# Performance work log

Hardware: AMD Instinct MI355X
Metric: run time of the kernel (lower is better)

The kernel has to match this reference:

```python
import jax, jax.numpy as jnp
import numpy as np

B, N = 16, 4096
N_IN, E_OUT = 128, 128          # inpt_dim[1], outp_dim[0]
OUT_N = 128                     # outp_dim[1]
G_DIM, CTXT_DIM = 64, 64
NODE_IN = E_OUT + N_IN          # 256, pre_ln size
CTXT_IN = G_DIM + CTXT_DIM      # 128
HID_F, HID_A = 256, 128
N_HEADS = 4
HEAD_DIM = OUT_N // N_HEADS     # 32
LN_EPS = 1e-5


def _init_w(key, fan_in, fan_out):
    return jax.random.normal(key, (fan_in, fan_out), jnp.float32) / np.float32(np.sqrt(fan_in))


def setup_inputs() -> dict:
    key = jax.random.key(0)
    ks = jax.random.split(key, 10)
    nodes = jax.random.normal(ks[0], (B, N, N_IN), jnp.float32)
    pooled_edges = jax.random.normal(ks[1], (B, N, E_OUT), jnp.float32)
    # variable-length graphs: valid prefix per graph (at least half the nodes)
    lengths = jax.random.randint(ks[2], (B,), N // 2, N + 1)
    mask = jnp.arange(N)[None, :] < lengths[:, None]
    globs = jax.random.normal(ks[3], (B, G_DIM), jnp.float32)
    ctxt = jax.random.normal(ks[4], (B, CTXT_DIM), jnp.float32)
    return {
        "nodes": nodes,
        "pooled_edges": pooled_edges,
        "mask": mask,
        "globs": globs,
        "ctxt": ctxt,
        "ln_g": jnp.ones((NODE_IN,), jnp.float32),
        "ln_b": jnp.zeros((NODE_IN,), jnp.float32),
        "feat_w1": _init_w(ks[5], NODE_IN + CTXT_IN, HID_F),
        "feat_b1": jnp.zeros((HID_F,), jnp.float32),
        "feat_w2": _init_w(ks[6], HID_F, OUT_N),
        "feat_b2": jnp.zeros((OUT_N,), jnp.float32),
        "attn_w1": _init_w(ks[7], NODE_IN + CTXT_IN, HID_A),
        "attn_b1": jnp.zeros((HID_A,), jnp.float32),
        "attn_w2": _init_w(ks[8], HID_A, N_HEADS),
        "attn_b2": jnp.zeros((N_HEADS,), jnp.float32),
    }


def _mlp(x, w1, b1, w2, b2):
    # DenseNetwork: one hidden block with LeakyReLU ("lrlu"), linear output
    h = jax.nn.leaky_relu(x @ w1 + b1)
    return h @ w2 + b2


def reference(nodes, pooled_edges, mask, globs, ctxt, ln_g, ln_b,
              feat_w1, feat_b1, feat_w2, feat_b2,
              attn_w1, attn_b1, attn_w2, attn_b2):
    # nodes = cat([graph.nodes, pooled_edges]) -> pre-LayerNorm
    x = jnp.concatenate([nodes, pooled_edges], axis=-1)           # [B,N,256]
    mu = jnp.mean(x, axis=-1, keepdims=True)
    var = jnp.var(x, axis=-1, keepdims=True)
    x = (x - mu) * jax.lax.rsqrt(var + LN_EPS) * ln_g + ln_b

    # high-level context broadcast to every node
    hl = jnp.concatenate([globs, ctxt], axis=-1)                   # [B,128]
    hl = jnp.broadcast_to(hl[:, None, :], (x.shape[0], x.shape[1], hl.shape[-1]))
    xin = jnp.concatenate([x, hl], axis=-1)                        # [B,N,384]

    # attention net with -inf padding, softmax over node axis (dim=-2)
    logits = _mlp(xin, attn_w1, attn_b1, attn_w2, attn_b2)          # [B,N,H]
    logits = jnp.where(mask[..., None], logits, -jnp.inf)
    w = jax.nn.softmax(logits, axis=1) / np.float32(np.sqrt(OUT_N))
    w = jnp.where(mask[..., None], w, 0.0)

    # feature net with 0 padding + residual (same_size)
    feats = _mlp(xin, feat_w1, feat_b1, feat_w2, feat_b2)           # [B,N,128]
    feats = jnp.where(mask[..., None], feats, 0.0)
    new_nodes = feats + nodes

    # expand per-head weights across head_dim, flatten, weighted node pooling
    w_full = jnp.repeat(w, HEAD_DIM, axis=-1)                       # [B,N,128]
    pooled = jnp.sum(new_nodes * w_full, axis=1)                    # [B,128]
    return (new_nodes, pooled)
```

## Files before the change

kernel.cpp:

```cpp
#include <hip/hip_runtime.h>
#include <stdint.h>

typedef unsigned short u16;
typedef unsigned char  u8;
typedef unsigned int   u32;
typedef __attribute__((ext_vector_type(8))) short bf16x8;
typedef __attribute__((ext_vector_type(4))) float f32x4;

static __device__ __forceinline__ float bf2f(u32 u) {
    union { u32 i; float f; } x; x.i = u << 16; return x.f;
}
static __device__ __forceinline__ u16 f2bf(float f) {
    union { u32 i; float f; } x; x.f = f;
    return (u16)((x.i + 0x7fffu + ((x.i >> 16) & 1u)) >> 16);
}
static __device__ __forceinline__ u32 packbf(float a, float b) {
    return (u32)f2bf(a) | ((u32)f2bf(b) << 16);
}
static __device__ __forceinline__ float ldf(const void* p, int i, int isf32) {
    return isf32 ? ((const float*)p)[i] : bf2f(((const u16*)p)[i]);
}
static __device__ __forceinline__ bool mvalid(const void* mask, int g, int mi32) {
    return mi32 ? (((const int*)mask)[g] != 0) : (((const u8*)mask)[g] != 0);
}

#define NTOT 65536
#define SXLD 264
#define SHLD 136
#define PVLD 144

__global__ __launch_bounds__(256) void k0_prep(
    const void* __restrict__ feat_w1, const void* __restrict__ attn_w1,
    const void* __restrict__ feat_b1, const void* __restrict__ attn_b1,
    const void* __restrict__ feat_w2, const void* __restrict__ attn_w2,
    const void* __restrict__ globs, const void* __restrict__ ctxt,
    const void* __restrict__ ln_g,
    u16* __restrict__ W1t, u16* __restrict__ W2t, u16* __restrict__ aw2t,
    float* __restrict__ hlc)
{
    __shared__ u16 tile[64][66];
    __shared__ float hl[128];
    const int isf32 = (((const u32*)ln_g)[0] == 0x3F800000u);
    const int bid = blockIdx.x;
    const int t = threadIdx.x;

    if (bid < 24) {
        int jt = bid >> 2, kt = bid & 3;
        int j0 = jt * 64, k0 = kt * 64;
        int jj = t & 63, kq = t >> 6;
#pragma unroll
        for (int r = 0; r < 16; r++) {
            int kk = r * 4 + kq;
            int j = j0 + jj;
            float v = (j < 256) ? ldf(feat_w1, (k0 + kk) * 256 + j, isf32)
                                : ldf(attn_w1, (k0 + kk) * 128 + (j - 256), isf32);
            tile[kk][jj] = f2bf(v);
        }
        __syncthreads();
        int kk2 = t & 63, jq = t >> 6;
#pragma unroll
        for (int r = 0; r < 16; r++) {
            int jj2 = r * 4 + jq;
            W1t[(size_t)(j0 + jj2) * 256 + k0 + kk2] = tile[kk2][jj2];
        }
    } else if (bid < 32) {
        int id2 = bid - 24;
        int ct2 = id2 >> 2, kt = id2 & 3;
        int c0 = ct2 * 64, k0 = kt * 64;
        int cc = t & 63, kq = t >> 6;
#pragma unroll
        for (int r = 0; r < 16; r++) {
            int kk = r * 4 + kq;
            tile[kk][cc] = f2bf(ldf(feat_w2, (k0 + kk) * 128 + c0 + cc, isf32));
        }
        __syncthreads();
        int kk2 = t & 63, cq = t >> 6;
#pragma unroll
        for (int r = 0; r < 16; r++) {
            int cc2 = r * 4 + cq;
            W2t[(size_t)(c0 + cc2) * 256 + k0 + kk2] = tile[kk2][cc2];
        }
    } else if (bid == 32) {
#pragma unroll
        for (int i = 0; i < 8; i++) {
            int e = i * 256 + t;
            int n = e >> 7, k = e & 127;
            aw2t[e] = (n < 4) ? f2bf(ldf(attn_w2, k * 4 + n, isf32)) : (u16)0;
        }
    } else {
        int b = bid - 33;
        if (t < 64)       hl[t] = ldf(globs, b * 64 + t, isf32);
        else if (t < 128) hl[t] = ldf(ctxt, b * 64 + (t - 64), isf32);
        __syncthreads();
        {
            float s = ldf(feat_b1, t, isf32);
#pragma unroll 8
            for (int c = 0; c < 128; c++)
                s += hl[c] * ldf(feat_w1, (256 + c) * 256 + t, isf32);
            hlc[b * 384 + t] = s;
        }
        if (t < 128) {
            float s = ldf(attn_b1, t, isf32);
#pragma unroll 8
            for (int c = 0; c < 128; c++)
                s += hl[c] * ldf(attn_w1, (256 + c) * 128 + t, isf32);
            hlc[b * 384 + 256 + t] = s;
        }
    }
}

__global__ __launch_bounds__(256, 3) void k_mega(
    const void* __restrict__ nodes, const void* __restrict__ edges,
    const void* __restrict__ ln_g, const void* __restrict__ ln_b,
    const u16* __restrict__ W1t, const u16* __restrict__ W2t,
    const u16* __restrict__ aw2t, const float* __restrict__ hlc,
    const void* __restrict__ attn_b2, const void* __restrict__ feat_b2,
    const void* __restrict__ mask,
    float* __restrict__ pv, void* __restrict__ outp)
{
    __shared__ __align__(16) u16 sX[64 * SXLD];
    __shared__ __align__(16) u16 sH[64 * SHLD];
    __shared__ float sG[256], sBt[256];
    __shared__ float sL[64][4];
    const int t = threadIdx.x;
    const int g0 = blockIdx.x * 64;
    const int b = g0 >> 12;
    const int isf32 = (((const u32*)ln_g)[0] == 0x3F800000u);
    const int mi32  = (((const u32*)mask)[0] == 1u);

    sG[t]  = ldf(ln_g, t, isf32);
    sBt[t] = ldf(ln_b, t, isf32);
    __syncthreads();

#pragma unroll
    for (int half = 0; half < 2; half++) {
        const int r = half * 32 + (t >> 3), q8 = t & 7;
        u32 pk[16];
#pragma unroll
        for (int j = 0; j < 4; j++) {
            int c = q8 + j * 8;
            if (isf32) {
                const float* src = (c < 16)
                    ? ((const float*)nodes + (size_t)(g0 + r) * 128 + c * 8)
                    : ((const float*)edges + (size_t)(g0 + r) * 128 + (c - 16) * 8);
                float4 v0 = ((const float4*)src)[0];
                float4 v1 = ((const float4*)src)[1];
                pk[4 * j]     = packbf(v0.x, v0.y);
                pk[4 * j + 1] = packbf(v0.z, v0.w);
                pk[4 * j + 2] = packbf(v1.x, v1.y);
                pk[4 * j + 3] = packbf(v1.z, v1.w);
            } else {
                const u16* src = (c < 16)
                    ? ((const u16*)nodes + (size_t)(g0 + r) * 128 + c * 8)
                    : ((const u16*)edges + (size_t)(g0 + r) * 128 + (c - 16) * 8);
                uint4 v = ((const uint4*)src)[0];
                pk[4 * j] = v.x; pk[4 * j + 1] = v.y;
                pk[4 * j + 2] = v.z; pk[4 * j + 3] = v.w;
            }
        }
        float s = 0.f, q = 0.f;
#pragma unroll
        for (int i = 0; i < 16; i++) {
            float lo = bf2f(pk[i] & 0xffffu), hi = bf2f(pk[i] >> 16);
            s += lo + hi; q += lo * lo + hi * hi;
        }
        s += __shfl_xor(s, 1, 64); s += __shfl_xor(s, 2, 64); s += __shfl_xor(s, 4, 64);
        q += __shfl_xor(q, 1, 64); q += __shfl_xor(q, 2, 64); q += __shfl_xor(q, 4, 64);
        float mu = s * (1.f / 256.f);
        float var = q * (1.f / 256.f) - mu * mu;
        float rs = rsqrtf(var + 1e-5f);
#pragma unroll
        for (int j = 0; j < 4; j++) {
            int c = q8 + j * 8;
            u32 ow[4];
#pragma unroll
            for (int k2 = 0; k2 < 4; k2++) {
                int col = c * 8 + k2 * 2;
                u32 w2 = pk[4 * j + k2];
                float y0 = (bf2f(w2 & 0xffffu) - mu) * rs * sG[col]     + sBt[col];
                float y1 = (bf2f(w2 >> 16)     - mu) * rs * sG[col + 1] + sBt[col + 1];
                ow[k2] = packbf(y0, y1);
            }
            *(uint4*)&sX[r * SXLD + c * 8] = make_uint4(ow[0], ow[1], ow[2], ow[3]);
        }
    }
    __syncthreads();

    const int w = t >> 6, l = t & 63;
    const int lr = l & 15, lq = l >> 4;
    const float ab2 = (lr < 4) ? ldf(attn_b2, lr, isf32) : 0.f;
    const float fb2_0 = ldf(feat_b2, w * 32 + lr, isf32);
    const float fb2_1 = ldf(feat_b2, w * 32 + 16 + lr, isf32);
    float* pvb = pv + (size_t)blockIdx.x * PVLD;

    f32x4 acc2[4][2];
#pragma unroll
    for (int rt = 0; rt < 4; rt++)
#pragma unroll
        for (int ct = 0; ct < 2; ct++) acc2[rt][ct] = (f32x4){0.f, 0.f, 0.f, 0.f};

    float nv[4][2][4];
    bool  mrow[4][4];

    const int order[3] = {2, 0, 1};
#pragma unroll
    for (int oi = 0; oi < 3; oi++) {
        const int nt = order[oi];

        float hbv[2];
#pragma unroll
        for (int ct = 0; ct < 2; ct++)
            hbv[ct] = hlc[b * 384 + nt * 128 + w * 32 + ct * 16 + lr];

        f32x4 acc1[4][2];
#pragma unroll
        for (int rt = 0; rt < 4; rt++)
#pragma unroll
            for (int ct = 0; ct < 2; ct++) acc1[rt][ct] = (f32x4){0.f, 0.f, 0.f, 0.f};

        const u16* Wp = W1t + (size_t)(nt * 128 + w * 32 + lr) * 256;
#pragma unroll
        for (int kh = 0; kh < 2; kh++) {
            bf16x8 bW[4][2];
#pragma unroll
            for (int kk = 0; kk < 4; kk++)
#pragma unroll
                for (int ct = 0; ct < 2; ct++)
                    bW[kk][ct] = *(const bf16x8*)(Wp + ct * 16 * 256 + (kh * 4 + kk) * 32 + lq * 8);
#pragma unroll
            for (int kk = 0; kk < 4; kk++) {
                bf16x8 aF[4];
#pragma unroll
                for (int rt = 0; rt < 4; rt++)
                    aF[rt] = *(const bf16x8*)&sX[(rt * 16 + lr) * SXLD + ((kh * 4 + kk) * 4 + lq) * 8];
#pragma unroll
                for (int rt = 0; rt < 4; rt++)
#pragma unroll
                    for (int ct = 0; ct < 2; ct++)
                        acc1[rt][ct] = __builtin_amdgcn_mfma_f32_16x16x32_bf16(aF[rt], bW[kk][ct], acc1[rt][ct], 0, 0, 0);
            }
        }

        __syncthreads();
#pragma unroll
        for (int rt = 0; rt < 4; rt++)
#pragma unroll
            for (int ct = 0; ct < 2; ct++)
#pragma unroll
                for (int reg = 0; reg < 4; reg++) {
                    int row = rt * 16 + lq * 4 + reg;
                    int col = w * 32 + ct * 16 + lr;
                    float hv = acc1[rt][ct][reg] + hbv[ct];
                    hv = (hv >= 0.f) ? hv : 0.01f * hv;
                    sH[row * SHLD + col] = f2bf(hv);
                }

        if (oi == 1) {
            const int row = l;
            const bool vld = mvalid(mask, g0 + row, mi32);
            float lg = sL[row][w];
            float x = vld ? lg : -1e30f;
#pragma unroll
            for (int o = 1; o < 64; o <<= 1) x = fmaxf(x, __shfl_xor(x, o, 64));
            float e = vld ? expf(lg - x) : 0.f;
            sL[row][w] = e;
            float sgm = e;
#pragma unroll
            for (int o = 1; o < 64; o <<= 1) sgm += __shfl_xor(sgm, o, 64);
            if (l == 0) { pvb[128 + w] = sgm; pvb[132 + w] = x; }
        }
        __syncthreads();

        if (nt == 2) {
            f32x4 accL = (f32x4){0.f, 0.f, 0.f, 0.f};
#pragma unroll
            for (int kk = 0; kk < 4; kk++) {
                bf16x8 aF = *(const bf16x8*)&sH[(w * 16 + lr) * SHLD + (kk * 4 + lq) * 8];
                bf16x8 bF = *(const bf16x8*)(aw2t + lr * 128 + kk * 32 + lq * 8);
                accL = __builtin_amdgcn_mfma_f32_16x16x32_bf16(aF, bF, accL, 0, 0, 0);
            }
            if (lr < 4) {
#pragma unroll
                for (int reg = 0; reg < 4; reg++)
                    sL[w * 16 + lq * 4 + reg][lr] = accL[reg] + ab2;
            }
        } else {
            if (oi == 2) {
#pragma unroll
                for (int rt = 0; rt < 4; rt++)
#pragma unroll
                    for (int reg = 0; reg < 4; reg++) {
                        int row = rt * 16 + lq * 4 + reg;
                        mrow[rt][reg] = mvalid(mask, g0 + row, mi32);
#pragma unroll
                        for (int ct = 0; ct < 2; ct++)
                            nv[rt][ct][reg] = ldf(nodes,
                                (g0 + row) * 128 + w * 32 + ct * 16 + lr, isf32);
                    }
            }
            const u16* W2p = W2t + (size_t)(w * 32 + lr) * 256 + nt * 128;
            bf16x8 bW2[4][2];
#pragma unroll
            for (int kk = 0; kk < 4; kk++)
#pragma unroll
                for (int ct = 0; ct < 2; ct++)
                    bW2[kk][ct] = *(const bf16x8*)(W2p + ct * 16 * 256 + kk * 32 + lq * 8);
#pragma unroll
            for (int kk = 0; kk < 4; kk++) {
                bf16x8 aF[4];
#pragma unroll
                for (int rt = 0; rt < 4; rt++)
                    aF[rt] = *(const bf16x8*)&sH[(rt * 16 + lr) * SHLD + (kk * 4 + lq) * 8];
#pragma unroll
                for (int rt = 0; rt < 4; rt++)
#pragma unroll
                    for (int ct = 0; ct < 2; ct++)
                        acc2[rt][ct] = __builtin_amdgcn_mfma_f32_16x16x32_bf16(aF[rt], bW2[kk][ct], acc2[rt][ct], 0, 0, 0);
            }
        }
    }

    float pc0 = 0.f, pc1 = 0.f;
#pragma unroll
    for (int rt = 0; rt < 4; rt++)
#pragma unroll
        for (int ct = 0; ct < 2; ct++)
#pragma unroll
            for (int reg = 0; reg < 4; reg++) {
                int row = rt * 16 + lq * 4 + reg;
                int col = w * 32 + ct * 16 + lr;
                int g = g0 + row;
                float v = acc2[rt][ct][reg] + (ct ? fb2_1 : fb2_0);
                v = mrow[rt][reg] ? v : 0.f;
                v += nv[rt][ct][reg];
                size_t idx = (size_t)g * 128 + col;
                if (isf32) ((float*)outp)[idx] = v;
                else       ((u16*)outp)[idx] = f2bf(v);
                float e = sL[row][w];
                if (ct) pc1 += e * v; else pc0 += e * v;
            }
    pc0 += __shfl_xor(pc0, 16, 64); pc0 += __shfl_xor(pc0, 32, 64);
    pc1 += __shfl_xor(pc1, 16, 64); pc1 += __shfl_xor(pc1, 32, 64);
    if (lq == 0) {
        pvb[w * 32 + lr]      = pc0;
        pvb[w * 32 + 16 + lr] = pc1;
    }
}

__global__ __launch_bounds__(256) void k_final(
    const float* __restrict__ pv, const void* __restrict__ ln_g,
    void* __restrict__ outbase)
{
    __shared__ float sm[64][4], ss[64][4], se[64][4];
    __shared__ float sZ[4];
    __shared__ float part[2][128];
    const int b = blockIdx.x;
    const int t = threadIdx.x;
    const int isf32 = (((const u32*)ln_g)[0] == 0x3F800000u);
    const float* pvb = pv + (size_t)b * 64 * PVLD;

#pragma unroll
    for (int i = t; i < 512; i += 256) {
        int rec = i >> 3, j = i & 7;
        float x = pvb[(size_t)rec * PVLD + 128 + j];
        if (j < 4) ss[rec][j] = x;
        else       sm[rec][j - 4] = x;
    }
    __syncthreads();

    {
        const int h = t >> 6, i = t & 63;
        float m = sm[i][h];
#pragma unroll
        for (int o = 1; o < 64; o <<= 1) m = fmaxf(m, __shfl_xor(m, o, 64));
        float e = expf(sm[i][h] - m);
        se[i][h] = e;
        float z = e * ss[i][h];
#pragma unroll
        for (int o = 1; o < 64; o <<= 1) z += __shfl_xor(z, o, 64);
        if (i == 0) sZ[h] = z;
    }
    __syncthreads();

    {
        const int c = t & 127, half = t >> 7;
        const int h = c >> 5;
        float acc = 0.f;
#pragma unroll 8
        for (int j = 0; j < 32; j++) {
            int rec = half * 32 + j;
            acc += se[rec][h] * pvb[(size_t)rec * PVLD + c];
        }
        part[half][c] = acc;
    }
    __syncthreads();
    if (t < 128) {
        float p = (part[0][t] + part[1][t]) * (0.08838834764831845f / sZ[t >> 5]);
        size_t off = (size_t)NTOT * 128 + (size_t)b * 128 + t;
        if (isf32) ((float*)outbase)[off] = p;
        else       ((u16*)outbase)[off] = f2bf(p);
    }
}

extern "C" void kernel_launch(void* const* d_in, const int* in_sizes, int n_in,
                              void* d_out, int out_size, void* d_ws, size_t ws_size,
                              hipStream_t stream)
{
    const void* nodes   = d_in[0];
    const void* edges   = d_in[1];
    const void* mask    = d_in[2];
    const void* globs   = d_in[3];
    const void* ctxt    = d_in[4];
    const void* ln_g    = d_in[5];
    const void* ln_b    = d_in[6];
    const void* feat_w1 = d_in[7];
    const void* feat_b1 = d_in[8];
    const void* feat_w2 = d_in[9];
    const void* feat_b2 = d_in[10];
    const void* attn_w1 = d_in[11];
    const void* attn_b1 = d_in[12];
    const void* attn_w2 = d_in[13];
    const void* attn_b2 = d_in[14];

    char* ws = (char*)d_ws;
    u16*   W1t    = (u16*)ws;   ws += (size_t)384 * 256 * 2;
    u16*   W2t    = (u16*)ws;   ws += (size_t)128 * 256 * 2;
    u16*   aw2t   = (u16*)ws;   ws += (size_t)16 * 128 * 2;
    float* hlc    = (float*)ws; ws += (size_t)16 * 384 * 4;
    float* pv     = (float*)ws; ws += (size_t)1024 * PVLD * 4;

    k0_prep <<<dim3(49),   dim3(256), 0, stream>>>(feat_w1, attn_w1, feat_b1, attn_b1,
                                                   feat_w2, attn_w2, globs, ctxt, ln_g,
                                                   W1t, W2t, aw2t, hlc);
    k_mega  <<<dim3(1024), dim3(256), 0, stream>>>(nodes, edges, ln_g, ln_b, W1t, W2t,
                                                   aw2t, hlc, attn_b2, feat_b2, mask,
                                                   pv, d_out);
    k_final <<<dim3(16),   dim3(256), 0, stream>>>(pv, ln_g, d_out);
}
```

Measured before the change: 198.0 us.

## Double waves per block and fold final pooling into last-arriving block

The main kernel now runs 512 threads per block with 8 waves, each owning 16 output columns instead of 32. This halves per-wave accumulator and weight-fragment registers, aiming for more latency hiding. The separate final reduction kernel is removed. The last block of each graph, found with an atomic counter and thread fences, now does the softmax-normalised pooling, saving one kernel launch. The cost is the atomic and fence overhead, a serial tail in the last block of each graph, and attention-logit MFMA work limited to half the waves.

```diff
diff --git a/kernel.cpp b/kernel.cpp
--- a/kernel.cpp
+++ b/kernel.cpp
@@ -36,7 +36,7 @@
     const void* __restrict__ globs, const void* __restrict__ ctxt,
     const void* __restrict__ ln_g,
     u16* __restrict__ W1t, u16* __restrict__ W2t, u16* __restrict__ aw2t,
-    float* __restrict__ hlc)
+    float* __restrict__ hlc, int* __restrict__ cnt)
 {
     __shared__ u16 tile[64][66];
     __shared__ float hl[128];
@@ -81,6 +81,7 @@
             W2t[(size_t)(c0 + cc2) * 256 + k0 + kk2] = tile[kk2][cc2];
         }
     } else if (bid == 32) {
+        if (t < 16) cnt[t] = 0;
 #pragma unroll
         for (int i = 0; i < 8; i++) {
             int e = i * 256 + t;
@@ -109,32 +110,31 @@
     }
 }
 
-__global__ __launch_bounds__(256, 3) void k_mega(
+__global__ __launch_bounds__(512, 4) void k_mega(
     const void* __restrict__ nodes, const void* __restrict__ edges,
     const void* __restrict__ ln_g, const void* __restrict__ ln_b,
     const u16* __restrict__ W1t, const u16* __restrict__ W2t,
     const u16* __restrict__ aw2t, const float* __restrict__ hlc,
     const void* __restrict__ attn_b2, const void* __restrict__ feat_b2,
     const void* __restrict__ mask,
-    float* __restrict__ pv, void* __restrict__ outp)
+    float* __restrict__ pv, int* __restrict__ cnt, void* __restrict__ outp)
 {
     __shared__ __align__(16) u16 sX[64 * SXLD];
     __shared__ __align__(16) u16 sH[64 * SHLD];
     __shared__ float sG[256], sBt[256];
     __shared__ float sL[64][4];
+    __shared__ int sFin;
     const int t = threadIdx.x;
     const int g0 = blockIdx.x * 64;
     const int b = g0 >> 12;
     const int isf32 = (((const u32*)ln_g)[0] == 0x3F800000u);
     const int mi32  = (((const u32*)mask)[0] == 1u);
 
-    sG[t]  = ldf(ln_g, t, isf32);
-    sBt[t] = ldf(ln_b, t, isf32);
-    __syncthreads();
-
-#pragma unroll
-    for (int half = 0; half < 2; half++) {
-        const int r = half * 32 + (t >> 3), q8 = t & 7;
+    if (t < 256) { sG[t] = ldf(ln_g, t, isf32); sBt[t] = ldf(ln_b, t, isf32); }
+    __syncthreads();
+
+    {
+        const int r = t >> 3, q8 = t & 7;
         u32 pk[16];
 #pragma unroll
         for (int j = 0; j < 4; j++) {
@@ -188,45 +188,35 @@
 
     const int w = t >> 6, l = t & 63;
     const int lr = l & 15, lq = l >> 4;
+    const int cb = w * 16;
     const float ab2 = (lr < 4) ? ldf(attn_b2, lr, isf32) : 0.f;
-    const float fb2_0 = ldf(feat_b2, w * 32 + lr, isf32);
-    const float fb2_1 = ldf(feat_b2, w * 32 + 16 + lr, isf32);
+    const float fb2 = ldf(feat_b2, cb + lr, isf32);
     float* pvb = pv + (size_t)blockIdx.x * PVLD;
 
-    f32x4 acc2[4][2];
-#pragma unroll
-    for (int rt = 0; rt < 4; rt++)
-#pragma unroll
-        for (int ct = 0; ct < 2; ct++) acc2[rt][ct] = (f32x4){0.f, 0.f, 0.f, 0.f};
-
-    float nv[4][2][4];
+    f32x4 acc2[4];
+#pragma unroll
+    for (int rt = 0; rt < 4; rt++) acc2[rt] = (f32x4){0.f, 0.f, 0.f, 0.f};
+
+    float nv[4][4];
     bool  mrow[4][4];
 
     const int order[3] = {2, 0, 1};
 #pragma unroll
     for (int oi = 0; oi < 3; oi++) {
         const int nt = order[oi];
-
-        float hbv[2];
-#pragma unroll
-        for (int ct = 0; ct < 2; ct++)
-            hbv[ct] = hlc[b * 384 + nt * 128 + w * 32 + ct * 16 + lr];
-
-        f32x4 acc1[4][2];
-#pragma unroll
-        for (int rt = 0; rt < 4; rt++)
-#pragma unroll
-            for (int ct = 0; ct < 2; ct++) acc1[rt][ct] = (f32x4){0.f, 0.f, 0.f, 0.f};
-
-        const u16* Wp = W1t + (size_t)(nt * 128 + w * 32 + lr) * 256;
+        const float hbv = hlc[b * 384 + nt * 128 + cb + lr];
+
+        f32x4 acc1[4];
+#pragma unroll
+        for (int rt = 0; rt < 4; rt++) acc1[rt] = (f32x4){0.f, 0.f, 0.f, 0.f};
+
+        const u16* Wp = W1t + (size_t)(nt * 128 + cb + lr) * 256;
 #pragma unroll
         for (int kh = 0; kh < 2; kh++) {
-            bf16x8 bW[4][2];
+            bf16x8 bW[4];
 #pragma unroll
             for (int kk = 0; kk < 4; kk++)
-#pragma unroll
-                for (int ct = 0; ct < 2; ct++)
-                    bW[kk][ct] = *(const bf16x8*)(Wp + ct * 16 * 256 + (kh * 4 + kk) * 32 + lq * 8);
+                bW[kk] = *(const bf16x8*)(Wp + (kh * 4 + kk) * 32 + lq * 8);
 #pragma unroll
             for (int kk = 0; kk < 4; kk++) {
                 bf16x8 aF[4];
@@ -235,9 +225,7 @@
                     aF[rt] = *(const bf16x8*)&sX[(rt * 16 + lr) * SXLD + ((kh * 4 + kk) * 4 + lq) * 8];
 #pragma unroll
                 for (int rt = 0; rt < 4; rt++)
-#pragma unroll
-                    for (int ct = 0; ct < 2; ct++)
-                        acc1[rt][ct] = __builtin_amdgcn_mfma_f32_16x16x32_bf16(aF[rt], bW[kk][ct], acc1[rt][ct], 0, 0, 0);
+                    acc1[rt] = __builtin_amdgcn_mfma_f32_16x16x32_bf16(aF[rt], bW[kk], acc1[rt], 0, 0, 0);
             }
         }
 
@@ -245,17 +233,14 @@
 #pragma unroll
         for (int rt = 0; rt < 4; rt++)
 #pragma unroll
-            for (int ct = 0; ct < 2; ct++)
-#pragma unroll
-                for (int reg = 0; reg < 4; reg++) {
-                    int row = rt * 16 + lq * 4 + reg;
-                    int col = w * 32 + ct * 16 + lr;
-                    float hv = acc1[rt][ct][reg] + hbv[ct];
-                    hv = (hv >= 0.f) ? hv : 0.01f * hv;
-                    sH[row * SHLD + col] = f2bf(hv);
-                }
-
-        if (oi == 1) {
+            for (int reg = 0; reg < 4; reg++) {
+                int row = rt * 16 + lq * 4 + reg;
+                float hv = acc1[rt][reg] + hbv;
+                hv = (hv >= 0.f) ? hv : 0.01f * hv;
+                sH[row * SHLD + cb + lr] = f2bf(hv);
+            }
+
+        if (oi == 1 && w < 4) {
             const int row = l;
             const bool vld = mvalid(mask, g0 + row, mi32);
             float lg = sL[row][w];
@@ -272,17 +257,19 @@
         __syncthreads();
 
         if (nt == 2) {
-            f32x4 accL = (f32x4){0.f, 0.f, 0.f, 0.f};
-#pragma unroll
-            for (int kk = 0; kk < 4; kk++) {
-                bf16x8 aF = *(const bf16x8*)&sH[(w * 16 + lr) * SHLD + (kk * 4 + lq) * 8];
-                bf16x8 bF = *(const bf16x8*)(aw2t + lr * 128 + kk * 32 + lq * 8);
-                accL = __builtin_amdgcn_mfma_f32_16x16x32_bf16(aF, bF, accL, 0, 0, 0);
-            }
-            if (lr < 4) {
-#pragma unroll
-                for (int reg = 0; reg < 4; reg++)
-                    sL[w * 16 + lq * 4 + reg][lr] = accL[reg] + ab2;
+            if (w < 4) {
+                f32x4 accL = (f32x4){0.f, 0.f, 0.f, 0.f};
+#pragma unroll
+                for (int kk = 0; kk < 4; kk++) {
+                    bf16x8 aF = *(const bf16x8*)&sH[(w * 16 + lr) * SHLD + (kk * 4 + lq) * 8];
+                    bf16x8 bF = *(const bf16x8*)(aw2t + lr * 128 + kk * 32 + lq * 8);
+                    accL = __builtin_amdgcn_mfma_f32_16x16x32_bf16(aF, bF, accL, 0, 0, 0);
+                }
+                if (lr < 4) {
+#pragma unroll
+                    for (int reg = 0; reg < 4; reg++)
+                        sL[w * 16 + lq * 4 + reg][lr] = accL[reg] + ab2;
+                }
             }
         } else {
             if (oi == 2) {
@@ -292,19 +279,14 @@
                     for (int reg = 0; reg < 4; reg++) {
                         int row = rt * 16 + lq * 4 + reg;
                         mrow[rt][reg] = mvalid(mask, g0 + row, mi32);
-#pragma unroll
-                        for (int ct = 0; ct < 2; ct++)
-                            nv[rt][ct][reg] = ldf(nodes,
-                                (g0 + row) * 128 + w * 32 + ct * 16 + lr, isf32);
+                        nv[rt][reg] = ldf(nodes, (g0 + row) * 128 + cb + lr, isf32);
                     }
             }
-            const u16* W2p = W2t + (size_t)(w * 32 + lr) * 256 + nt * 128;
-            bf16x8 bW2[4][2];
+            const u16* W2p = W2t + (size_t)(cb + lr) * 256 + nt * 128;
+            bf16x8 bW2[4];
 #pragma unroll
             for (int kk = 0; kk < 4; kk++)
-#pragma unroll
-                for (int ct = 0; ct < 2; ct++)
-                    bW2[kk][ct] = *(const bf16x8*)(W2p + ct * 16 * 256 + kk * 32 + lq * 8);
+                bW2[kk] = *(const bf16x8*)(W2p + kk * 32 + lq * 8);
 #pragma unroll
             for (int kk = 0; kk < 4; kk++) {
                 bf16x8 aF[4];
@@ -313,92 +295,82 @@
                     aF[rt] = *(const bf16x8*)&sH[(rt * 16 + lr) * SHLD + (kk * 4 + lq) * 8];
 #pragma unroll
                 for (int rt = 0; rt < 4; rt++)
-#pragma unroll
-                    for (int ct = 0; ct < 2; ct++)
-                        acc2[rt][ct] = __builtin_amdgcn_mfma_f32_16x16x32_bf16(aF[rt], bW2[kk][ct], acc2[rt][ct], 0, 0, 0);
-            }
-        }
-    }
-
-    float pc0 = 0.f, pc1 = 0.f;
+                    acc2[rt] = __builtin_amdgcn_mfma_f32_16x16x32_bf16(aF[rt], bW2[kk], acc2[rt], 0, 0, 0);
+            }
+        }
+    }
+
+    float pc = 0.f;
 #pragma unroll
     for (int rt = 0; rt < 4; rt++)
 #pragma unroll
-        for (int ct = 0; ct < 2; ct++)
-#pragma unroll
-            for (int reg = 0; reg < 4; reg++) {
-                int row = rt * 16 + lq * 4 + reg;
-                int col = w * 32 + ct * 16 + lr;
-                int g = g0 + row;
-                float v = acc2[rt][ct][reg] + (ct ? fb2_1 : fb2_0);
-                v = mrow[rt][reg] ? v : 0.f;
-                v += nv[rt][ct][reg];
-                size_t idx = (size_t)g * 128 + col;
-                if (isf32) ((float*)outp)[idx] = v;
-                else       ((u16*)outp)[idx] = f2bf(v);
-                float e = sL[row][w];
-                if (ct) pc1 += e * v; else pc0 += e * v;
-            }
-    pc0 += __shfl_xor(pc0, 16, 64); pc0 += __shfl_xor(pc0, 32, 64);
-    pc1 += __shfl_xor(pc1, 16, 64); pc1 += __shfl_xor(pc1, 32, 64);
-    if (lq == 0) {
-        pvb[w * 32 + lr]      = pc0;
-        pvb[w * 32 + 16 + lr] = pc1;
-    }
-}
-
-__global__ __launch_bounds__(256) void k_final(
-    const float* __restrict__ pv, const void* __restrict__ ln_g,
-    void* __restrict__ outbase)
-{
-    __shared__ float sm[64][4], ss[64][4], se[64][4];
-    __shared__ float sZ[4];
-    __shared__ float part[2][128];
-    const int b = blockIdx.x;
-    const int t = threadIdx.x;
-    const int isf32 = (((const u32*)ln_g)[0] == 0x3F800000u);
-    const float* pvb = pv + (size_t)b * 64 * PVLD;
-
-#pragma unroll
-    for (int i = t; i < 512; i += 256) {
-        int rec = i >> 3, j = i & 7;
-        float x = pvb[(size_t)rec * PVLD + 128 + j];
-        if (j < 4) ss[rec][j] = x;
-        else       sm[rec][j - 4] = x;
-    }
-    __syncthreads();
+        for (int reg = 0; reg < 4; reg++) {
+            int row = rt * 16 + lq * 4 + reg;
+            int g = g0 + row;
+            float v = acc2[rt][reg] + fb2;
+            v = mrow[rt][reg] ? v : 0.f;
+            v += nv[rt][reg];
+            size_t idx = (size_t)g * 128 + cb + lr;
+            if (isf32) ((float*)outp)[idx] = v;
+            else       ((u16*)outp)[idx] = f2bf(v);
+            pc += sL[row][w >> 1] * v;
+        }
+    pc += __shfl_xor(pc, 16, 64); pc += __shfl_xor(pc, 32, 64);
+    if (lq == 0) pvb[cb + lr] = pc;
+
+    __threadfence();
+    if (t == 0) sFin = (atomicAdd(&cnt[b], 1) == 63);
+    __syncthreads();
+    if (!sFin) return;
+    __threadfence();
+
+    float* fsm  = (float*)sX;
+    float* fss  = fsm + 256;
+    float* fse  = fss + 256;
+    float* fsZ  = fse + 256;
+    float* fpart = fsZ + 4;
+    const float* pvbase = pv + (size_t)(b * 64) * PVLD;
 
     {
+        int rec = t >> 3, j = t & 7;
+        float x = pvbase[(size_t)rec * PVLD + 128 + j];
+        if (j < 4) fss[rec * 4 + j] = x;
+        else       fsm[rec * 4 + (j - 4)] = x;
+    }
+    __syncthreads();
+
+    if (t < 256) {
         const int h = t >> 6, i = t & 63;
-        float m = sm[i][h];
+        float m = fsm[i * 4 + h];
 #pragma unroll
         for (int o = 1; o < 64; o <<= 1) m = fmaxf(m, __shfl_xor(m, o, 64));
-        float e = expf(sm[i][h] - m);
-        se[i][h] = e;
-        float z = e * ss[i][h];
+        float e = expf(fsm[i * 4 + h] - m);
+        fse[i * 4 + h] = e;
+        float z = e * fss[i * 4 + h];
 #pragma unroll
         for (int o = 1; o < 64; o <<= 1) z += __shfl_xor(z, o, 64);
-        if (i == 0) sZ[h] = z;
+        if (i == 0) fsZ[h] = z;
     }
     __syncthreads();
 
     {
-        const int c = t & 127, half = t >> 7;
+        const int c = t & 127, qq = t >> 7;
         const int h = c >> 5;
         float acc = 0.f;
-#pragma unroll 8
-        for (int j = 0; j < 32; j++) {
-            int rec = half * 32 + j;
-            acc += se[rec][h] * pvb[(size_t)rec * PVLD + c];
-        }
-        part[half][c] = acc;
+#pragma unroll
+        for (int j = 0; j < 16; j++) {
+            int rec = qq * 16 + j;
+            acc += fse[rec * 4 + h] * pvbase[(size_t)rec * PVLD + c];
+        }
+        fpart[qq * 128 + c] = acc;
     }
     __syncthreads();
     if (t < 128) {
-        float p = (part[0][t] + part[1][t]) * (0.08838834764831845f / sZ[t >> 5]);
+        float p = (fpart[t] + fpart[128 + t] + fpart[256 + t] + fpart[384 + t])
+                  * (0.08838834764831845f / fsZ[t >> 5]);
         size_t off = (size_t)NTOT * 128 + (size_t)b * 128 + t;
-        if (isf32) ((float*)outbase)[off] = p;
-        else       ((u16*)outbase)[off] = f2bf(p);
+        if (isf32) ((float*)outp)[off] = p;
+        else       ((u16*)outp)[off] = f2bf(p);
     }
 }
 
@@ -428,12 +400,12 @@
     u16*   aw2t   = (u16*)ws;   ws += (size_t)16 * 128 * 2;
     float* hlc    = (float*)ws; ws += (size_t)16 * 384 * 4;
     float* pv     = (float*)ws; ws += (size_t)1024 * PVLD * 4;
+    int*   cnt    = (int*)ws;   ws += 16 * 4;
 
     k0_prep <<<dim3(49),   dim3(256), 0, stream>>>(feat_w1, attn_w1, feat_b1, attn_b1,
                                                    feat_w2, attn_w2, globs, ctxt, ln_g,
-                                                   W1t, W2t, aw2t, hlc);
-    k_mega  <<<dim3(1024), dim3(256), 0, stream>>>(nodes, edges, ln_g, ln_b, W1t, W2t,
+                                                   W1t, W2t, aw2t, hlc, cnt);
+    k_mega  <<<dim3(1024), dim3(512), 0, stream>>>(nodes, edges, ln_g, ln_b, W1t, W2t,
                                                    aw2t, hlc, attn_b2, feat_b2, mask,
-                                                   pv, d_out);
-    k_final <<<dim3(16),   dim3(256), 0, stream>>>(pv, ln_g, d_out);
-}
+                                                   pv, cnt, d_out);
+}
```

Measured after the change: 454.0 us. 129% more time.

## Prefetch next W1 tile before barrier and split final pooling per head

Applied to the files above, without the earlier changes.

The main kernel now issues global loads of the first half of each W1 column block before the LayerNorm barrier and prefetches the next block's first half while the current block finishes, so weight-fetch latency overlaps with MFMA work and the barrier. The final reduction kernel is split into 64 blocks (one per batch and head) instead of 16, which spreads the softmax-combine work across more CUs. This raises register pressure in the mega kernel because of the extra prefetched fragments, which could cut occupancy.

```diff
diff --git a/kernel.cpp b/kernel.cpp
--- a/kernel.cpp
+++ b/kernel.cpp
@@ -184,7 +184,6 @@
             *(uint4*)&sX[r * SXLD + c * 8] = make_uint4(ow[0], ow[1], ow[2], ow[3]);
         }
     }
-    __syncthreads();
 
     const int w = t >> 6, l = t & 63;
     const int lr = l & 15, lq = l >> 4;
@@ -193,6 +192,17 @@
     const float fb2_1 = ldf(feat_b2, w * 32 + 16 + lr, isf32);
     float* pvb = pv + (size_t)blockIdx.x * PVLD;
 
+    bf16x8 bW0[4][2];
+    {
+        const u16* Wf = W1t + (size_t)(2 * 128 + w * 32 + lr) * 256;
+#pragma unroll
+        for (int kk = 0; kk < 4; kk++)
+#pragma unroll
+            for (int ct = 0; ct < 2; ct++)
+                bW0[kk][ct] = *(const bf16x8*)(Wf + ct * 16 * 256 + kk * 32 + lq * 8);
+    }
+    __syncthreads();
+
     f32x4 acc2[4][2];
 #pragma unroll
     for (int rt = 0; rt < 4; rt++)
@@ -219,26 +229,47 @@
             for (int ct = 0; ct < 2; ct++) acc1[rt][ct] = (f32x4){0.f, 0.f, 0.f, 0.f};
 
         const u16* Wp = W1t + (size_t)(nt * 128 + w * 32 + lr) * 256;
-#pragma unroll
-        for (int kh = 0; kh < 2; kh++) {
-            bf16x8 bW[4][2];
+
+#pragma unroll
+        for (int kk = 0; kk < 4; kk++) {
+            bf16x8 aF[4];
+#pragma unroll
+            for (int rt = 0; rt < 4; rt++)
+                aF[rt] = *(const bf16x8*)&sX[(rt * 16 + lr) * SXLD + (kk * 4 + lq) * 8];
+#pragma unroll
+            for (int rt = 0; rt < 4; rt++)
+#pragma unroll
+                for (int ct = 0; ct < 2; ct++)
+                    acc1[rt][ct] = __builtin_amdgcn_mfma_f32_16x16x32_bf16(aF[rt], bW0[kk][ct], acc1[rt][ct], 0, 0, 0);
+        }
+        {
+            bf16x8 bW1[4][2];
 #pragma unroll
             for (int kk = 0; kk < 4; kk++)
 #pragma unroll
                 for (int ct = 0; ct < 2; ct++)
-                    bW[kk][ct] = *(const bf16x8*)(Wp + ct * 16 * 256 + (kh * 4 + kk) * 32 + lq * 8);
+                    bW1[kk][ct] = *(const bf16x8*)(Wp + ct * 16 * 256 + (4 + kk) * 32 + lq * 8);
 #pragma unroll
             for (int kk = 0; kk < 4; kk++) {
                 bf16x8 aF[4];
 #pragma unroll
                 for (int rt = 0; rt < 4; rt++)
-                    aF[rt] = *(const bf16x8*)&sX[(rt * 16 + lr) * SXLD + ((kh * 4 + kk) * 4 + lq) * 8];
+                    aF[rt] = *(const bf16x8*)&sX[(rt * 16 + lr) * SXLD + ((4 + kk) * 4 + lq) * 8];
 #pragma unroll
                 for (int rt = 0; rt < 4; rt++)
 #pragma unroll
                     for (int ct = 0; ct < 2; ct++)
-                        acc1[rt][ct] = __builtin_amdgcn_mfma_f32_16x16x32_bf16(aF[rt], bW[kk][ct], acc1[rt][ct], 0, 0, 0);
-            }
+                        acc1[rt][ct] = __builtin_amdgcn_mfma_f32_16x16x32_bf16(aF[rt], bW1[kk][ct], acc1[rt][ct], 0, 0, 0);
+            }
+        }
+
+        if (oi < 2) {
+            const u16* Wn = W1t + (size_t)(order[oi + 1] * 128 + w * 32 + lr) * 256;
+#pragma unroll
+            for (int kk = 0; kk < 4; kk++)
+#pragma unroll
+                for (int ct = 0; ct < 2; ct++)
+                    bW0[kk][ct] = *(const bf16x8*)(Wn + ct * 16 * 256 + kk * 32 + lq * 8);
         }
 
         __syncthreads();
@@ -351,52 +382,54 @@
     const float* __restrict__ pv, const void* __restrict__ ln_g,
     void* __restrict__ outbase)
 {
-    __shared__ float sm[64][4], ss[64][4], se[64][4];
-    __shared__ float sZ[4];
-    __shared__ float part[2][128];
-    const int b = blockIdx.x;
+    __shared__ float sm[64], ss[64], se[64];
+    __shared__ float sZ;
+    __shared__ float part[8][32];
+    const int blk = blockIdx.x;
+    const int b = blk >> 2, q = blk & 3;
     const int t = threadIdx.x;
     const int isf32 = (((const u32*)ln_g)[0] == 0x3F800000u);
     const float* pvb = pv + (size_t)b * 64 * PVLD;
 
-#pragma unroll
-    for (int i = t; i < 512; i += 256) {
-        int rec = i >> 3, j = i & 7;
-        float x = pvb[(size_t)rec * PVLD + 128 + j];
-        if (j < 4) ss[rec][j] = x;
-        else       sm[rec][j - 4] = x;
+    if (t < 128) {
+        int rec = t >> 1, j = t & 1;
+        float x = pvb[(size_t)rec * PVLD + 128 + j * 4 + q];
+        if (j == 0) ss[rec] = x;
+        else        sm[rec] = x;
     }
     __syncthreads();
 
+    if (t < 64) {
+        float m = sm[t];
+#pragma unroll
+        for (int o = 1; o < 64; o <<= 1) m = fmaxf(m, __shfl_xor(m, o, 64));
+        float e = expf(sm[t] - m);
+        se[t] = e;
+        float z = e * ss[t];
+#pragma unroll
+        for (int o = 1; o < 64; o <<= 1) z += __shfl_xor(z, o, 64);
+        if (t == 0) sZ = z;
+    }
+    __syncthreads();
+
     {
-        const int h = t >> 6, i = t & 63;
-        float m = sm[i][h];
-#pragma unroll
-        for (int o = 1; o < 64; o <<= 1) m = fmaxf(m, __shfl_xor(m, o, 64));
-        float e = expf(sm[i][h] - m);
-        se[i][h] = e;
-        float z = e * ss[i][h];
-#pragma unroll
-        for (int o = 1; o < 64; o <<= 1) z += __shfl_xor(z, o, 64);
-        if (i == 0) sZ[h] = z;
+        const int ci = t & 31, rg = t >> 5;
+        const int c = q * 32 + ci;
+        float acc = 0.f;
+#pragma unroll
+        for (int j = 0; j < 8; j++) {
+            int rec = rg * 8 + j;
+            acc += se[rec] * pvb[(size_t)rec * PVLD + c];
+        }
+        part[rg][ci] = acc;
     }
     __syncthreads();
-
-    {
-        const int c = t & 127, half = t >> 7;
-        const int h = c >> 5;
-        float acc = 0.f;
-#pragma unroll 8
-        for (int j = 0; j < 32; j++) {
-            int rec = half * 32 + j;
-            acc += se[rec][h] * pvb[(size_t)rec * PVLD + c];
-        }
-        part[half][c] = acc;
-    }
-    __syncthreads();
-    if (t < 128) {
-        float p = (part[0][t] + part[1][t]) * (0.08838834764831845f / sZ[t >> 5]);
-        size_t off = (size_t)NTOT * 128 + (size_t)b * 128 + t;
+    if (t < 32) {
+        float s = 0.f;
+#pragma unroll
+        for (int r = 0; r < 8; r++) s += part[r][t];
+        float p = s * (0.08838834764831845f / sZ);
+        size_t off = (size_t)NTOT * 128 + (size_t)b * 128 + q * 32 + t;
         if (isf32) ((float*)outbase)[off] = p;
         else       ((u16*)outbase)[off] = f2bf(p);
     }
@@ -435,5 +468,5 @@
     k_mega  <<<dim3(1024), dim3(256), 0, stream>>>(nodes, edges, ln_g, ln_b, W1t, W2t,
                                                    aw2t, hlc, attn_b2, feat_b2, mask,
                                                    pv, d_out);
-    k_final <<<dim3(16),   dim3(256), 0, stream>>>(pv, ln_g, d_out);
-}
+    k_final <<<dim3(64),   dim3(256), 0, stream>>>(pv, ln_g, d_out);
+}
```

Result: no change. 197.4 us (-0.3%).
